# Kernel tuning notes

Measured on AMD Instinct MI355X. Metric: run time of the kernel, lower is better.

## Reference

```python
import jax, jax.numpy as jnp
import numpy as np


def setup_inputs() -> dict:
    key = jax.random.key(0)
    k1, k2, k3, k4, k5 = jax.random.split(key, 5)
    B, S, DK, D = 64, 2048, 1024, 1024
    hidden_state = jax.random.normal(k1, (B, D), dtype=jnp.float32)
    encoder_outputs = jax.random.normal(k2, (B, S, DK), dtype=jnp.float32)
    # linear1: in = dim_key + dim*num_layers = 2048, out = dim = 1024
    W1 = jax.random.normal(k3, (D, DK + D), dtype=jnp.float32) * (1.0 / np.sqrt(DK + D))
    b1 = jax.random.normal(k4, (D,), dtype=jnp.float32) * 0.01
    W2 = jax.random.normal(k5, (1, D), dtype=jnp.float32) * (1.0 / np.sqrt(D))
    return {"hidden_state": hidden_state, "encoder_outputs": encoder_outputs,
            "W1": W1, "b1": b1, "W2": W2}


def reference(hidden_state, encoder_outputs, W1, b1, W2):
    # torch: cat([enc, h], -1) @ W1.T  ==  enc @ W1e.T + h @ W1h.T
    # (split avoids materializing the [B,S,DK+D] concat; same math)
    DK = encoder_outputs.shape[-1]
    W1e, W1h = W1[:, :DK], W1[:, DK:]
    # pre: [B, S, D]
    pre = (jnp.einsum('bsk,dk->bsd', encoder_outputs, W1e)
           + jnp.einsum('bm,dm->bd', hidden_state, W1h)[:, None, :]
           + b1)
    e = jnp.einsum('bsd,d->bs', jnp.tanh(pre), W2[0])  # scores [B, S]
    alpha = jax.nn.softmax(e, axis=1)
    context = jnp.einsum('bs,bsk->bk', alpha, encoder_outputs)  # [B, DK]
    return context
```

## Files before the change

### kernel.cpp

```cpp
#include <hip/hip_runtime.h>

typedef __attribute__((ext_vector_type(8))) short short8;
typedef __attribute__((ext_vector_type(4))) float floatx4;

#define M_TOT 131072
#define SEQ   2048
#define NB    8

__device__ __forceinline__ unsigned bf16rne(float x) {
  unsigned u = __float_as_uint(x);
  return (u + 0x7FFFu + ((u >> 16) & 1u)) >> 16;
}

#define GLOAD_LDS16(g, l) __builtin_amdgcn_global_load_lds( \
    (const __attribute__((address_space(1))) unsigned int*)(g), \
    (__attribute__((address_space(3))) unsigned int*)(l), 16, 0, 0)

__global__ __launch_bounds__(256) void convert_enc_frag_kernel(
    const float* __restrict__ in, unsigned int* __restrict__ out)
{
  unsigned C = blockIdx.x * 256 + threadIdx.x;
  int l = C & 63, mt = (C >> 6) & 3, wm = (C >> 8) & 3;
  int t = (C >> 10) & 31, mb = C >> 15;
  int row = mb * 256 + wm * 64 + mt * 16 + (l & 15);
  int k0  = t * 32 + (l >> 4) * 8;
  const float* p = in + (size_t)row * 1024 + k0;
  float4 a = *(const float4*)p;
  float4 b = *(const float4*)(p + 4);
  uint4 o;
  o.x = bf16rne(a.x) | (bf16rne(a.y) << 16);
  o.y = bf16rne(a.z) | (bf16rne(a.w) << 16);
  o.z = bf16rne(b.x) | (bf16rne(b.y) << 16);
  o.w = bf16rne(b.z) | (bf16rne(b.w) << 16);
  *(uint4*)(out + (size_t)C * 4) = o;
}

__global__ __launch_bounds__(256) void convert_w1e_frag_kernel(
    const float* __restrict__ W1, unsigned int* __restrict__ out)
{
  unsigned G = blockIdx.x * 256 + threadIdx.x;
  int l = G & 63, nt = (G >> 6) & 3, wn = (G >> 8) & 1;
  int t = (G >> 9) & 31, nb = G >> 14;
  int d  = nb * 128 + wn * 64 + nt * 16 + (l & 15);
  int k0 = t * 32 + (l >> 4) * 8;
  const float* p = W1 + (size_t)d * 2048 + k0;
  float4 a = *(const float4*)p;
  float4 b = *(const float4*)(p + 4);
  uint4 o;
  o.x = bf16rne(a.x) | (bf16rne(a.y) << 16);
  o.y = bf16rne(a.z) | (bf16rne(a.w) << 16);
  o.z = bf16rne(b.x) | (bf16rne(b.y) << 16);
  o.w = bf16rne(b.z) | (bf16rne(b.w) << 16);
  *(uint4*)(out + (size_t)G * 4) = o;
}

__global__ __launch_bounds__(256) void hvec_kernel(
    const float* __restrict__ hid, const float* __restrict__ W1,
    const float* __restrict__ b1, float* __restrict__ hvec)
{
  int b = blockIdx.x, g = blockIdx.y;
  int w = threadIdx.x >> 6, lane = threadIdx.x & 63;
  const float* hrow = hid + b * 1024;
  for (int i = 0; i < 4; ++i) {
    int d = g * 16 + w * 4 + i;
    const float* wrow = W1 + (size_t)d * 2048 + 1024;
    float sum = 0.f;
#pragma unroll
    for (int c = 0; c < 4; ++c) {
      int m = c * 256 + lane * 4;
      float4 wv = *(const float4*)(wrow + m);
      float4 hv = *(const float4*)(hrow + m);
      sum += wv.x * hv.x + wv.y * hv.y + wv.z * hv.z + wv.w * hv.w;
    }
#pragma unroll
    for (int msk = 1; msk < 64; msk <<= 1) sum += __shfl_xor(sum, msk);
    if (lane == 0) hvec[b * 1024 + d] = sum + b1[d];
  }
}

__global__ __launch_bounds__(512, 4) void gemm256x128_kernel(
    const unsigned short* __restrict__ encB, const unsigned short* __restrict__ W1eB,
    const float* __restrict__ W2, const float* __restrict__ hvec,
    float* __restrict__ epart)
{
  __shared__ __align__(16) unsigned short ldsA[3][8192];
  __shared__ __align__(16) unsigned short ldsB[3][4096];

  const int tid = threadIdx.x;
  const int lid = blockIdx.x;
  const int xcd = lid & 7, q = lid >> 3;
  const int mb = xcd * 64 + (q >> 3);
  const int nb = q & 7;
  const int r0 = mb * 256;
  const int bidx = mb >> 3;
  const int wid = tid >> 6, lane = tid & 63;
  const int wm = wid >> 1, wn = wid & 1;
  const int lrow = lane & 15, kq = lane >> 4;
  const int lane8 = lane * 8;

  floatx4 acc[4][4];
#pragma unroll
  for (int i = 0; i < 4; ++i)
#pragma unroll
    for (int j = 0; j < 4; ++j)
      acc[i][j] = (floatx4){0.f, 0.f, 0.f, 0.f};

  unsigned short *aCur = ldsA[0], *aNx = ldsA[1], *aN2 = ldsA[2];
  unsigned short *bCur = ldsB[0], *bNx = ldsB[1], *bN2 = ldsB[2];

  {
    const unsigned short* ga = encB + ((size_t)mb * 32 * 1024 + tid) * 8;
    GLOAD_LDS16(ga,        &aCur[wid * 512]);
    GLOAD_LDS16(ga + 4096, &aCur[4096 + wid * 512]);
    const unsigned short* gb = W1eB + ((size_t)nb * 32 * 512 + tid) * 8;
    GLOAD_LDS16(gb,        &bCur[wid * 512]);
  }

  const int aRd = wm * 2048 + lane8;
  const int bRd = wn * 2048 + lane8;

  for (int t = 0; t < 32; ++t) {
    if (t < 31) {
      const unsigned short* ga = encB + ((size_t)(mb * 32 + t + 1) * 1024 + tid) * 8;
      GLOAD_LDS16(ga,        &aNx[wid * 512]);
      GLOAD_LDS16(ga + 4096, &aNx[4096 + wid * 512]);
      const unsigned short* gb = W1eB + ((size_t)(nb * 32 + t + 1) * 512 + tid) * 8;
      GLOAD_LDS16(gb,        &bNx[wid * 512]);
      asm volatile("s_waitcnt vmcnt(3)" ::: "memory");
    } else {
      asm volatile("s_waitcnt vmcnt(0)" ::: "memory");
    }
    __builtin_amdgcn_s_barrier();

    short8 af[4], bf[4];
#pragma unroll
    for (int mt = 0; mt < 4; ++mt) af[mt] = *(const short8*)&aCur[aRd + mt * 512];
#pragma unroll
    for (int nt = 0; nt < 4; ++nt) bf[nt] = *(const short8*)&bCur[bRd + nt * 512];
    __builtin_amdgcn_s_setprio(1);
#pragma unroll
    for (int mt = 0; mt < 4; ++mt)
#pragma unroll
      for (int nt = 0; nt < 4; ++nt)
        acc[mt][nt] = __builtin_amdgcn_mfma_f32_16x16x32_bf16(
            af[mt], bf[nt], acc[mt][nt], 0, 0, 0);
    __builtin_amdgcn_s_setprio(0);

    unsigned short* tA = aCur; aCur = aNx; aNx = aN2; aN2 = tA;
    unsigned short* tB = bCur; bCur = bNx; bNx = bN2; bN2 = tB;
  }

  __syncthreads();
  float* ep = (float*)&ldsA[0][0];
  float hv[4], w2v[4];
#pragma unroll
  for (int nt = 0; nt < 4; ++nt) {
    int n = nb * 128 + wn * 64 + nt * 16 + lrow;
    hv[nt]  = hvec[bidx * 1024 + n];
    w2v[nt] = W2[n];
  }
#pragma unroll
  for (int mt = 0; mt < 4; ++mt) {
#pragma unroll
    for (int r = 0; r < 4; ++r) {
      float sum = 0.f;
#pragma unroll
      for (int nt = 0; nt < 4; ++nt) {
        float pre = acc[mt][nt][r] + hv[nt];
        float ex = __expf(2.f * pre);
        sum += (1.f - 2.f / (ex + 1.f)) * w2v[nt];
      }
      sum += __shfl_xor(sum, 1);
      sum += __shfl_xor(sum, 2);
      sum += __shfl_xor(sum, 4);
      sum += __shfl_xor(sum, 8);
      if (lrow == 0) ep[wn * 256 + wm * 64 + mt * 16 + kq * 4 + r] = sum;
    }
  }
  __syncthreads();
  if (tid < 256)
    epart[(size_t)nb * M_TOT + r0 + tid] = ep[tid] + ep[256 + tid];
}

__global__ __launch_bounds__(256) void fused_gemm_kernel(
    const float* __restrict__ enc, const float* __restrict__ W1,
    const float* __restrict__ W2, const float* __restrict__ hvec,
    float* __restrict__ epart)
{
  __shared__ __align__(16) unsigned short Ah[128 * 32];
  __shared__ __align__(16) unsigned short Bh[128 * 32];
  __shared__ float ep[2][128];

  const int tid = threadIdx.x;
  const int nb = blockIdx.x, mb = blockIdx.y;
  const int r0 = mb * 128, n0 = nb * 128;
  const int bidx = r0 >> 11;
  const int w = tid >> 6, lane = tid & 63;
  const int wm = w >> 1, wn = w & 1;
  const int lrow = lane & 15, kq = lane >> 4;

  floatx4 acc[4][4];
#pragma unroll
  for (int i = 0; i < 4; ++i)
#pragma unroll
    for (int j = 0; j < 4; ++j)
      acc[i][j] = (floatx4){0.f, 0.f, 0.f, 0.f};

  const int srow = tid >> 3;
  const int scol = (tid & 7) * 4;
  const float* aptr = enc + (size_t)(r0 + srow) * 1024 + scol;
  const float* bptr = W1  + (size_t)(n0 + srow) * 2048 + scol;

  for (int k0 = 0; k0 < 1024; k0 += 32) {
    float4 av[4], bv[4];
#pragma unroll
    for (int j = 0; j < 4; ++j) {
      av[j] = *(const float4*)(aptr + (size_t)(j * 32) * 1024 + k0);
      bv[j] = *(const float4*)(bptr + (size_t)(j * 32) * 2048 + k0);
    }
    __syncthreads();
#pragma unroll
    for (int j = 0; j < 4; ++j) {
      unsigned ax = __float_as_uint(av[j].x), ay = __float_as_uint(av[j].y);
      unsigned az = __float_as_uint(av[j].z), aw = __float_as_uint(av[j].w);
      unsigned a01 = __builtin_amdgcn_perm(ay, ax, 0x07060302u);
      unsigned a23 = __builtin_amdgcn_perm(aw, az, 0x07060302u);
      *(uint2*)&Ah[(tid + j * 256) * 4] = make_uint2(a01, a23);
      unsigned bx = __float_as_uint(bv[j].x), by = __float_as_uint(bv[j].y);
      unsigned bz = __float_as_uint(bv[j].z), bw = __float_as_uint(bv[j].w);
      unsigned b01 = __builtin_amdgcn_perm(by, bx, 0x07060302u);
      unsigned b23 = __builtin_amdgcn_perm(bw, bz, 0x07060302u);
      *(uint2*)&Bh[(tid + j * 256) * 4] = make_uint2(b01, b23);
    }
    __syncthreads();

    short8 af[4], bfm[4];
#pragma unroll
    for (int t4 = 0; t4 < 4; ++t4) {
      af[t4]  = *(const short8*)&Ah[(wm * 64 + t4 * 16 + lrow) * 32 + kq * 8];
      bfm[t4] = *(const short8*)&Bh[(wn * 64 + t4 * 16 + lrow) * 32 + kq * 8];
    }
#pragma unroll
    for (int mt = 0; mt < 4; ++mt)
#pragma unroll
      for (int nt = 0; nt < 4; ++nt)
        acc[mt][nt] = __builtin_amdgcn_mfma_f32_16x16x32_bf16(
            af[mt], bfm[nt], acc[mt][nt], 0, 0, 0);
  }

  float hv[4], w2v[4];
#pragma unroll
  for (int nt = 0; nt < 4; ++nt) {
    int n = n0 + wn * 64 + nt * 16 + lrow;
    hv[nt]  = hvec[bidx * 1024 + n];
    w2v[nt] = W2[n];
  }
#pragma unroll
  for (int mt = 0; mt < 4; ++mt) {
#pragma unroll
    for (int r = 0; r < 4; ++r) {
      float sum = 0.f;
#pragma unroll
      for (int nt = 0; nt < 4; ++nt) {
        float pre = acc[mt][nt][r] + hv[nt];
        float ex = __expf(2.f * pre);
        sum += (1.f - 2.f / (ex + 1.f)) * w2v[nt];
      }
      sum += __shfl_xor(sum, 1);
      sum += __shfl_xor(sum, 2);
      sum += __shfl_xor(sum, 4);
      sum += __shfl_xor(sum, 8);
      if (lrow == 0) ep[wn][wm * 64 + mt * 16 + kq * 4 + r] = sum;
    }
  }
  __syncthreads();
  if (tid < 128)
    epart[(size_t)nb * M_TOT + r0 + tid] = ep[0][tid] + ep[1][tid];
}

__global__ __launch_bounds__(256) void softmax_kernel(
    const float* __restrict__ epart, float* __restrict__ alpha)
{
  int b = blockIdx.x, t = threadIdx.x;
  __shared__ float redmax[4], redsum[4];
  float ev[8];
  float lmax = -1e30f;
#pragma unroll
  for (int j = 0; j < 8; ++j) {
    int s = t + j * 256;
    float sum = 0.f;
#pragma unroll
    for (int p = 0; p < 8; ++p) sum += epart[(size_t)p * M_TOT + b * SEQ + s];
    ev[j] = sum;
    lmax = fmaxf(lmax, sum);
  }
#pragma unroll
  for (int msk = 1; msk < 64; msk <<= 1) lmax = fmaxf(lmax, __shfl_xor(lmax, msk));
  if ((t & 63) == 0) redmax[t >> 6] = lmax;
  __syncthreads();
  float bmax = fmaxf(fmaxf(redmax[0], redmax[1]), fmaxf(redmax[2], redmax[3]));
  float lsum = 0.f;
#pragma unroll
  for (int j = 0; j < 8; ++j) { ev[j] = __expf(ev[j] - bmax); lsum += ev[j]; }
#pragma unroll
  for (int msk = 1; msk < 64; msk <<= 1) lsum += __shfl_xor(lsum, msk);
  if ((t & 63) == 0) redsum[t >> 6] = lsum;
  __syncthreads();
  float inv = 1.f / (redsum[0] + redsum[1] + redsum[2] + redsum[3]);
#pragma unroll
  for (int j = 0; j < 8; ++j) alpha[b * SEQ + t + j * 256] = ev[j] * inv;
}

__global__ __launch_bounds__(512) void context_f32_kernel(
    const float* __restrict__ enc, const float* __restrict__ alpha,
    float* __restrict__ out)
{
  __shared__ float red[16][128];
  int b = blockIdx.x, kc = blockIdx.y, t = threadIdx.x;
  int kl = (t & 31) * 4;
  int strip = t >> 5;
  const float* ep = enc + ((size_t)b * SEQ + strip * 128) * 1024 + kc * 128 + kl;
  const float* ap = alpha + b * SEQ + strip * 128;
  float a0 = 0.f, a1 = 0.f, a2 = 0.f, a3 = 0.f;
#pragma unroll 4
  for (int s = 0; s < 128; ++s) {
    float a = ap[s];
    float4 v = *(const float4*)(ep + (size_t)s * 1024);
    a0 += a * v.x; a1 += a * v.y; a2 += a * v.z; a3 += a * v.w;
  }
  red[strip][kl + 0] = a0;
  red[strip][kl + 1] = a1;
  red[strip][kl + 2] = a2;
  red[strip][kl + 3] = a3;
  __syncthreads();
  if (t < 128) {
    float s = 0.f;
#pragma unroll
    for (int j = 0; j < 16; ++j) s += red[j][t];
    out[b * 1024 + kc * 128 + t] = s;
  }
}

__global__ __launch_bounds__(256) void context_kernel(
    const float* __restrict__ enc, const float* __restrict__ alpha,
    float* __restrict__ out)
{
  int b = blockIdx.y, sq = blockIdx.z, t = threadIdx.x;
  int k4 = t * 4;
  const float* ep = enc + ((size_t)b * SEQ + sq * 128) * 1024 + k4;
  const float* ap = alpha + b * SEQ + sq * 128;
  float ax = 0.f, ay = 0.f, az = 0.f, aw = 0.f;
#pragma unroll 4
  for (int s = 0; s < 128; ++s) {
    float a = ap[s];
    float4 v = *(const float4*)(ep + (size_t)s * 1024);
    ax += a * v.x; ay += a * v.y; az += a * v.z; aw += a * v.w;
  }
  float* o = out + b * 1024 + k4;
  atomicAdd(o + 0, ax);
  atomicAdd(o + 1, ay);
  atomicAdd(o + 2, az);
  atomicAdd(o + 3, aw);
}

extern "C" void kernel_launch(void* const* d_in, const int* in_sizes, int n_in,
                              void* d_out, int out_size, void* d_ws, size_t ws_size,
                              hipStream_t stream) {
  const float* hid = (const float*)d_in[0];
  const float* enc = (const float*)d_in[1];
  const float* W1  = (const float*)d_in[2];
  const float* b1  = (const float*)d_in[3];
  const float* W2  = (const float*)d_in[4];
  float* out = (float*)d_out;

  float* epart = (float*)d_ws;
  float* alpha = epart + (size_t)NB * M_TOT;
  float* hvec  = alpha + M_TOT;
  size_t small_bytes = ((size_t)NB * M_TOT + M_TOT + 64 * 1024) * 4;
  size_t encB_off = ((small_bytes + 255) / 256) * 256;
  size_t need = encB_off + (size_t)M_TOT * 1024 * 2 + (size_t)1024 * 1024 * 2;

  hvec_kernel<<<dim3(64, 64), 256, 0, stream>>>(hid, W1, b1, hvec);

  if (ws_size >= need) {
    unsigned short* encB = (unsigned short*)((char*)d_ws + encB_off);
    unsigned short* W1eB = encB + (size_t)M_TOT * 1024;
    convert_enc_frag_kernel<<<65536, 256, 0, stream>>>(enc, (unsigned int*)encB);
    convert_w1e_frag_kernel<<<512, 256, 0, stream>>>(W1, (unsigned int*)W1eB);
    gemm256x128_kernel<<<4096, 512, 0, stream>>>(encB, W1eB, W2, hvec, epart);
    softmax_kernel<<<64, 256, 0, stream>>>(epart, alpha);
    context_f32_kernel<<<dim3(64, 8), 512, 0, stream>>>(enc, alpha, out);
  } else {
    hipMemsetAsync(d_out, 0, (size_t)out_size * sizeof(float), stream);
    fused_gemm_kernel<<<dim3(NB, 1024), 256, 0, stream>>>(enc, W1, W2, hvec, epart);
    softmax_kernel<<<64, 256, 0, stream>>>(epart, alpha);
    context_kernel<<<dim3(1, 64, 16), 256, 0, stream>>>(enc, alpha, out);
  }
}
```

Baseline: 1.137 ms.

## Fuse fp32-to-bf16 encoder conversion into GEMM A-tile staging

Removes the separate pass that converted the encoder outputs to a bf16 fragment layout in workspace. The GEMM now loads fp32 encoder rows into registers one tile ahead, converts them with packed bf16 instructions and writes them into the LDS ring, while B tiles still use direct global-to-LDS loads. This avoids writing and rereading a 256MB bf16 copy. In exchange the GEMM reads twice the A bytes as fp32 (the N-blocks each reread the same encoder rows), carries more register pressure, and has more complex wait-count synchronization.

```diff
diff --git a/kernel.cpp b/kernel.cpp
--- a/kernel.cpp
+++ b/kernel.cpp
@@ -12,28 +12,15 @@
   return (u + 0x7FFFu + ((u >> 16) & 1u)) >> 16;
 }
 
+__device__ __forceinline__ unsigned cvtpk_bf16(float lo, float hi) {
+  unsigned r;
+  asm("v_cvt_pk_bf16_f32 %0, %1, %2" : "=v"(r) : "v"(lo), "v"(hi));
+  return r;
+}
+
 #define GLOAD_LDS16(g, l) __builtin_amdgcn_global_load_lds( \
     (const __attribute__((address_space(1))) unsigned int*)(g), \
     (__attribute__((address_space(3))) unsigned int*)(l), 16, 0, 0)
-
-__global__ __launch_bounds__(256) void convert_enc_frag_kernel(
-    const float* __restrict__ in, unsigned int* __restrict__ out)
-{
-  unsigned C = blockIdx.x * 256 + threadIdx.x;
-  int l = C & 63, mt = (C >> 6) & 3, wm = (C >> 8) & 3;
-  int t = (C >> 10) & 31, mb = C >> 15;
-  int row = mb * 256 + wm * 64 + mt * 16 + (l & 15);
-  int k0  = t * 32 + (l >> 4) * 8;
-  const float* p = in + (size_t)row * 1024 + k0;
-  float4 a = *(const float4*)p;
-  float4 b = *(const float4*)(p + 4);
-  uint4 o;
-  o.x = bf16rne(a.x) | (bf16rne(a.y) << 16);
-  o.y = bf16rne(a.z) | (bf16rne(a.w) << 16);
-  o.z = bf16rne(b.x) | (bf16rne(b.y) << 16);
-  o.w = bf16rne(b.z) | (bf16rne(b.w) << 16);
-  *(uint4*)(out + (size_t)C * 4) = o;
-}
 
 __global__ __launch_bounds__(256) void convert_w1e_frag_kernel(
     const float* __restrict__ W1, unsigned int* __restrict__ out)
@@ -78,8 +65,8 @@
   }
 }
 
-__global__ __launch_bounds__(512, 4) void gemm256x128_kernel(
-    const unsigned short* __restrict__ encB, const unsigned short* __restrict__ W1eB,
+__global__ __launch_bounds__(512, 4) void gemm_fused_kernel(
+    const float* __restrict__ enc, const unsigned short* __restrict__ W1eB,
     const float* __restrict__ W2, const float* __restrict__ hvec,
     float* __restrict__ epart)
 {
@@ -98,6 +85,15 @@
   const int lrow = lane & 15, kq = lane >> 4;
   const int lane8 = lane * 8;
 
+  const float* aSrc[2];
+  int aDst[2];
+#pragma unroll
+  for (int j = 0; j < 2; ++j) {
+    int c = tid + j * 512, row = c >> 2, kc = c & 3;
+    aSrc[j] = enc + (size_t)(r0 + row) * 1024 + kc * 8;
+    aDst[j] = ((row >> 4) * 64 + (row & 15) + kc * 16) * 8;
+  }
+
   floatx4 acc[4][4];
 #pragma unroll
   for (int i = 0; i < 4; ++i)
@@ -105,38 +101,59 @@
     for (int j = 0; j < 4; ++j)
       acc[i][j] = (floatx4){0.f, 0.f, 0.f, 0.f};
 
-  unsigned short *aCur = ldsA[0], *aNx = ldsA[1], *aN2 = ldsA[2];
-  unsigned short *bCur = ldsB[0], *bNx = ldsB[1], *bN2 = ldsB[2];
-
-  {
-    const unsigned short* ga = encB + ((size_t)mb * 32 * 1024 + tid) * 8;
-    GLOAD_LDS16(ga,        &aCur[wid * 512]);
-    GLOAD_LDS16(ga + 4096, &aCur[4096 + wid * 512]);
-    const unsigned short* gb = W1eB + ((size_t)nb * 32 * 512 + tid) * 8;
-    GLOAD_LDS16(gb,        &bCur[wid * 512]);
-  }
+  float4 aR[2][2];
+#define LOAD_AR(T) do { \
+    _Pragma("unroll") \
+    for (int j = 0; j < 2; ++j) { \
+      aR[j][0] = *(const float4*)(aSrc[j] + (T) * 32); \
+      aR[j][1] = *(const float4*)(aSrc[j] + (T) * 32 + 4); \
+    } \
+  } while (0)
+#define CVT_WRITE_A(SL) do { \
+    _Pragma("unroll") \
+    for (int j = 0; j < 2; ++j) { \
+      uint4 o; \
+      o.x = cvtpk_bf16(aR[j][0].x, aR[j][0].y); \
+      o.y = cvtpk_bf16(aR[j][0].z, aR[j][0].w); \
+      o.z = cvtpk_bf16(aR[j][1].x, aR[j][1].y); \
+      o.w = cvtpk_bf16(aR[j][1].z, aR[j][1].w); \
+      *(uint4*)&ldsA[SL][aDst[j]] = o; \
+    } \
+  } while (0)
+#define STAGE_B(T, SL) \
+    GLOAD_LDS16(W1eB + ((size_t)(nb * 32 + (T)) * 512 + tid) * 8, \
+                &ldsB[SL][wid * 512])
+
+  LOAD_AR(0);
+  STAGE_B(0, 0);
+  CVT_WRITE_A(0);
+  LOAD_AR(1);
 
   const int aRd = wm * 2048 + lane8;
   const int bRd = wn * 2048 + lane8;
 
+  int sCur = 0;
   for (int t = 0; t < 32; ++t) {
+    const int sNx = (sCur == 2) ? 0 : sCur + 1;
     if (t < 31) {
-      const unsigned short* ga = encB + ((size_t)(mb * 32 + t + 1) * 1024 + tid) * 8;
-      GLOAD_LDS16(ga,        &aNx[wid * 512]);
-      GLOAD_LDS16(ga + 4096, &aNx[4096 + wid * 512]);
-      const unsigned short* gb = W1eB + ((size_t)(nb * 32 + t + 1) * 512 + tid) * 8;
-      GLOAD_LDS16(gb,        &bNx[wid * 512]);
-      asm volatile("s_waitcnt vmcnt(3)" ::: "memory");
+      CVT_WRITE_A(sNx);
+      if (t < 30) LOAD_AR(t + 2);
+      STAGE_B(t + 1, sNx);
+      asm volatile("s_waitcnt lgkmcnt(0)" ::: "memory");
+      if (t < 30) { asm volatile("s_waitcnt vmcnt(5)" ::: "memory"); }
+      else        { asm volatile("s_waitcnt vmcnt(1)" ::: "memory"); }
     } else {
-      asm volatile("s_waitcnt vmcnt(0)" ::: "memory");
+      asm volatile("s_waitcnt vmcnt(0) lgkmcnt(0)" ::: "memory");
     }
     __builtin_amdgcn_s_barrier();
 
     short8 af[4], bf[4];
 #pragma unroll
-    for (int mt = 0; mt < 4; ++mt) af[mt] = *(const short8*)&aCur[aRd + mt * 512];
-#pragma unroll
-    for (int nt = 0; nt < 4; ++nt) bf[nt] = *(const short8*)&bCur[bRd + nt * 512];
+    for (int mt = 0; mt < 4; ++mt)
+      af[mt] = *(const short8*)&ldsA[sCur][aRd + mt * 512];
+#pragma unroll
+    for (int nt = 0; nt < 4; ++nt)
+      bf[nt] = *(const short8*)&ldsB[sCur][bRd + nt * 512];
     __builtin_amdgcn_s_setprio(1);
 #pragma unroll
     for (int mt = 0; mt < 4; ++mt)
@@ -146,9 +163,11 @@
             af[mt], bf[nt], acc[mt][nt], 0, 0, 0);
     __builtin_amdgcn_s_setprio(0);
 
-    unsigned short* tA = aCur; aCur = aNx; aNx = aN2; aN2 = tA;
-    unsigned short* tB = bCur; bCur = bNx; bNx = bN2; bN2 = tB;
-  }
+    sCur = sNx;
+  }
+#undef LOAD_AR
+#undef CVT_WRITE_A
+#undef STAGE_B
 
   __syncthreads();
   float* ep = (float*)&ldsA[0][0];
@@ -377,17 +396,15 @@
   float* alpha = epart + (size_t)NB * M_TOT;
   float* hvec  = alpha + M_TOT;
   size_t small_bytes = ((size_t)NB * M_TOT + M_TOT + 64 * 1024) * 4;
-  size_t encB_off = ((small_bytes + 255) / 256) * 256;
-  size_t need = encB_off + (size_t)M_TOT * 1024 * 2 + (size_t)1024 * 1024 * 2;
+  size_t w1eb_off = ((small_bytes + 255) / 256) * 256;
+  size_t need = w1eb_off + (size_t)1024 * 1024 * 2;
 
   hvec_kernel<<<dim3(64, 64), 256, 0, stream>>>(hid, W1, b1, hvec);
 
   if (ws_size >= need) {
-    unsigned short* encB = (unsigned short*)((char*)d_ws + encB_off);
-    unsigned short* W1eB = encB + (size_t)M_TOT * 1024;
-    convert_enc_frag_kernel<<<65536, 256, 0, stream>>>(enc, (unsigned int*)encB);
+    unsigned short* W1eB = (unsigned short*)((char*)d_ws + w1eb_off);
     convert_w1e_frag_kernel<<<512, 256, 0, stream>>>(W1, (unsigned int*)W1eB);
-    gemm256x128_kernel<<<4096, 512, 0, stream>>>(encB, W1eB, W2, hvec, epart);
+    gemm_fused_kernel<<<4096, 512, 0, stream>>>(enc, W1eB, W2, hvec, epart);
     softmax_kernel<<<64, 256, 0, stream>>>(epart, alpha);
     context_f32_kernel<<<dim3(64, 8), 512, 0, stream>>>(enc, alpha, out);
   } else {
```

After: 1.078 ms. -5.3%, faster.
